# Kernel optimization log

Hardware: AMD Instinct MI355X
Metric: run time of the kernel (lower is better)

The kernel has to match this reference:

```python
import jax, jax.numpy as jnp
import numpy as np

B, C, T, F = 256, 1, 8192, 16


def _lrelu(h):
    return jnp.where(h > 0, h, 0.01 * h)


def _adain(h, style):
    # h: (B, T, 8), style: (B, 8, 2)
    scale = style[:, None, :, 0]          # (B, 1, 8)
    bias = style[:, None, :, 1]           # (B, 1, 8)
    mu = jnp.mean(h, axis=-1, keepdims=True)
    sigma = jnp.std(h, axis=-1, ddof=1, keepdims=True) + 1e-6  # torch.std is unbiased
    return scale * (h - mu) / sigma + bias


def setup_inputs() -> dict:
    key = jax.random.key(0)
    ks = jax.random.split(key, 20)
    g = lambda k, shp, s=0.2: (jax.random.normal(k, shp, dtype=jnp.float32) * s)
    inp = {
        "x": jax.random.normal(ks[0], (B, C, T), dtype=jnp.float32),
        "metadata": jax.random.normal(ks[1], (B, F), dtype=jnp.float32),
        # MetadataMLP: F->64->128->64 (total_channels*2 = 32*2)
        "mw1": g(ks[2], (F, 64)), "mb1": g(ks[3], (64,)),
        "mw2": g(ks[4], (64, 128)), "mb2": g(ks[5], (128,)),
        "mw3": g(ks[6], (128, 64)), "mb3": g(ks[7], (64,)),
        # main chain 1->8->8->8->8->1
        "w1": g(ks[8], (1, 8)), "b1": g(ks[9], (8,)),
        "w2": g(ks[10], (8, 8)), "b2": g(ks[11], (8,)),
        "w3": g(ks[12], (8, 8)), "b3": g(ks[13], (8,)),
        "w4": g(ks[14], (8, 8)), "b4": g(ks[15], (8,)),
        "w5": g(ks[16], (8, 1)), "b5": g(ks[17], (1,)),
    }
    return inp


def reference(x, metadata, mw1, mb1, mw2, mb2, mw3, mb3,
              w1, b1, w2, b2, w3, b3, w4, b4, w5, b5):
    # style MLP
    s = jax.nn.relu(metadata @ mw1 + mb1)
    s = jax.nn.relu(s @ mw2 + mb2)
    s = s @ mw3 + mb3                     # (B, 64)
    s1, s2, s3, s4 = jnp.split(s, 4, axis=1)  # each (B, 16)
    s1, s2, s3, s4 = (t.reshape(-1, 8, 2) for t in (s1, s2, s3, s4))

    h = jnp.transpose(x, (0, 2, 1))       # (B, T, 1)
    h = h @ w1 + b1                       # (B, T, 8)
    h = _lrelu(_adain(h, s1))
    h = h @ w2 + b2
    h = _lrelu(_adain(h, s2))
    h = h @ w3 + b3
    h = _lrelu(_adain(h, s3))
    h = h @ w4 + b4
    h = _lrelu(_adain(h, s4))
    h = h @ w5 + b5                       # (B, T, 1)
    out = _lrelu(h)
    return jnp.transpose(out, (0, 2, 1))  # (B, 1, T)
```

## Files before the change

kernel.cpp:

```cpp
#include <hip/hip_runtime.h>

#define BATCH   256
#define TLEN    8192
#define TPB     256
#define EPT     2
#define CHUNKS  (TLEN / (TPB * EPT))
#define PSTRIDE 320
#define SQRT7   2.6457513110645906f
#define C1      2.6457513110645906e-6f


__device__ __forceinline__ float rowmean8(const float* __restrict__ p) {
    return (((p[0] + p[1]) + (p[2] + p[3])) + ((p[4] + p[5]) + (p[6] + p[7]))) * 0.125f;
}

__device__ __forceinline__ float lrelu(float t) { return fmaxf(t, 0.01f * t); }

__global__ __launch_bounds__(128) void prep_kernel(
    const float* __restrict__ metadata,
    const float* __restrict__ mw1, const float* __restrict__ mb1,
    const float* __restrict__ mw2, const float* __restrict__ mb2,
    const float* __restrict__ mw3, const float* __restrict__ mb3,
    const float* __restrict__ w1, const float* __restrict__ b1,
    const float* __restrict__ w2, const float* __restrict__ b2,
    const float* __restrict__ w3, const float* __restrict__ b3,
    const float* __restrict__ w4, const float* __restrict__ b4,
    const float* __restrict__ w5, const float* __restrict__ b5,
    float* __restrict__ P)
{
    const int b   = blockIdx.x;
    const int tid = threadIdx.x;
    __shared__ float md[16];
    __shared__ float h1[64];
    __shared__ float h2[128];
    __shared__ float s[64];
    __shared__ float la[8], lc[8];

    if (tid < 16) md[tid] = metadata[b * 16 + tid];
    __syncthreads();

    if (tid < 64) {
        float a = mb1[tid];
        #pragma unroll
        for (int k = 0; k < 16; ++k) a = fmaf(md[k], mw1[k * 64 + tid], a);
        h1[tid] = fmaxf(a, 0.f);
    }
    __syncthreads();

    {
        float a = mb2[tid];
        #pragma unroll 16
        for (int k = 0; k < 64; ++k) a = fmaf(h1[k], mw2[k * 128 + tid], a);
        h2[tid] = fmaxf(a, 0.f);
    }
    __syncthreads();

    if (tid < 64) {
        float a = mb3[tid];
        #pragma unroll 16
        for (int k = 0; k < 128; ++k) a = fmaf(h2[k], mw3[k * 64 + tid], a);
        s[tid] = a;
    }
    if (tid >= 64 && tid < 72) {
        int j = tid - 64;
        la[j] = w1[j] - rowmean8(w1);
        lc[j] = b1[j] - rowmean8(b1);
    }
    __syncthreads();

    float* __restrict__ p = P + b * PSTRIDE;

    if (tid == 0) {
        float A = 0.f, B = 0.f, C = 0.f;
        #pragma unroll
        for (int j = 0; j < 8; ++j) {
            A = fmaf(la[j], la[j], A);
            B = fmaf(la[j], lc[j], B);
            C = fmaf(lc[j], lc[j], C);
        }
        p[24] = A; p[25] = 2.f * B; p[26] = C; p[27] = b5[0];
    }
    if (tid < 8) {
        const float sc1 = s[2 * tid] * SQRT7;
        p[tid]      = la[tid] * sc1;
        p[8 + tid]  = lc[tid] * sc1;
        p[16 + tid] = s[2 * tid + 1];
        p[32 + 64 + tid]  = b2[tid] - rowmean8(b2);
        p[32 + 72 + tid]  = s[16 + 2 * tid] * SQRT7;
        p[32 + 80 + tid]  = s[16 + 2 * tid + 1];
        p[120 + 64 + tid] = b3[tid] - rowmean8(b3);
        p[120 + 72 + tid] = s[32 + 2 * tid] * SQRT7;
        p[120 + 80 + tid] = s[32 + 2 * tid + 1];
        p[208 + 64 + tid] = b4[tid] - rowmean8(b4);
        p[208 + 72 + tid] = s[48 + 2 * tid] * SQRT7;
        p[208 + 80 + tid] = s[48 + 2 * tid + 1];
        p[296 + tid]      = w5[tid];
    }
    if (tid >= 64) {
        int i = tid - 64;
        p[32 + i]  = w2[i] - rowmean8(w2 + (i & 56));
        p[120 + i] = w3[i] - rowmean8(w3 + (i & 56));
        p[208 + i] = w4[i] - rowmean8(w4 + (i & 56));
    }
}

__global__ __launch_bounds__(TPB, 6) void adain_main_kernel(
    const float* __restrict__ x, const float* __restrict__ P, float* __restrict__ out)
{
    const int tid   = threadIdx.x;
    const int b     = blockIdx.x / CHUNKS;
    const int chunk = blockIdx.x % CHUNKS;

    const float* __restrict__ p = P + b * PSTRIDE;

    const float cA = p[24], cB2 = p[25], cC = p[26], lb5 = p[27];

    const int i2 = b * (TLEN / 2) + chunk * TPB + tid;
    const float2 v2 = ((const float2*)x)[i2];
    const float ve[2] = {v2.x, v2.y};
    float h[2][8];

    #pragma unroll
    for (int e = 0; e < 2; ++e) {
        const float var = fmaxf(fmaf(ve[e], fmaf(ve[e], cA, cB2), cC), 0.f);
        const float r   = __builtin_amdgcn_rcpf(__builtin_amdgcn_sqrtf(var) + C1);
        #pragma unroll
        for (int j = 0; j < 8; ++j) {
            const float d = fmaf(ve[e], p[j], p[8 + j]);
            h[e][j] = lrelu(fmaf(d, r, p[16 + j]));
        }
    }

    #pragma unroll
    for (int l = 0; l < 3; ++l) {
        const float* __restrict__ w = p + 32 + l * 88;

        float cbv[8], sbv[8];
        #pragma unroll
        for (int j = 0; j < 8; ++j) { cbv[j] = w[64 + j]; sbv[j] = w[80 + j]; }

        float g[2][8];
        #pragma unroll
        for (int e = 0; e < 2; ++e)
            #pragma unroll
            for (int j = 0; j < 8; ++j)
                g[e][j] = fmaf(h[e][0], w[j], cbv[j]);

        #pragma unroll
        for (int k = 1; k < 8; ++k)
            #pragma unroll
            for (int e = 0; e < 2; ++e)
                #pragma unroll
                for (int j = 0; j < 8; ++j)
                    g[e][j] = fmaf(h[e][k], w[k * 8 + j], g[e][j]);

        #pragma unroll
        for (int e = 0; e < 2; ++e) {
            float var = 0.f;
            #pragma unroll
            for (int j = 0; j < 8; ++j) var = fmaf(g[e][j], g[e][j], var);
            const float r = __builtin_amdgcn_rcpf(__builtin_amdgcn_sqrtf(var) + C1);
            #pragma unroll
            for (int j = 0; j < 8; ++j)
                h[e][j] = lrelu(fmaf(g[e][j] * r, w[72 + j], sbv[j]));
        }
    }

    float oe[2];
    #pragma unroll
    for (int e = 0; e < 2; ++e) {
        float a = lb5;
        #pragma unroll
        for (int k = 0; k < 8; ++k) a = fmaf(h[e][k], p[296 + k], a);
        oe[e] = lrelu(a);
    }
    ((float2*)out)[i2] = make_float2(oe[0], oe[1]);
}

extern "C" void kernel_launch(void* const* d_in, const int* in_sizes, int n_in,
                              void* d_out, int out_size, void* d_ws, size_t ws_size,
                              hipStream_t stream)
{
    const float* x        = (const float*)d_in[0];
    const float* metadata = (const float*)d_in[1];
    const float* mw1      = (const float*)d_in[2];
    const float* mb1      = (const float*)d_in[3];
    const float* mw2      = (const float*)d_in[4];
    const float* mb2      = (const float*)d_in[5];
    const float* mw3      = (const float*)d_in[6];
    const float* mb3      = (const float*)d_in[7];
    const float* w1       = (const float*)d_in[8];
    const float* b1       = (const float*)d_in[9];
    const float* w2       = (const float*)d_in[10];
    const float* b2       = (const float*)d_in[11];
    const float* w3       = (const float*)d_in[12];
    const float* b3       = (const float*)d_in[13];
    const float* w4       = (const float*)d_in[14];
    const float* b4       = (const float*)d_in[15];
    const float* w5       = (const float*)d_in[16];
    const float* b5       = (const float*)d_in[17];

    float* P = (float*)d_ws;

    prep_kernel<<<BATCH, 128, 0, stream>>>(
        metadata, mw1, mb1, mw2, mb2, mw3, mb3,
        w1, b1, w2, b2, w3, b3, w4, b4, w5, b5, P);
    adain_main_kernel<<<BATCH * CHUNKS, TPB, 0, stream>>>(x, P, (float*)d_out);
}
```

Baseline: 118.2 us.

## Stage per-batch params in LDS and process four elements per thread

Each thread now handles four timesteps loaded as a float4 instead of two. The per-batch parameter block is copied into shared memory once per block, and the weights are read as vectorized LDS loads. The layer loop is no longer unrolled and the occupancy hint drops from 6 to 4 blocks. The aim is fewer scalar/global parameter loads per element and wider memory transactions, at the cost of a block barrier, higher register pressure and fewer blocks in the grid.

```diff
diff --git a/kernel.cpp b/kernel.cpp
--- a/kernel.cpp
+++ b/kernel.cpp
@@ -3,7 +3,7 @@
 #define BATCH   256
 #define TLEN    8192
 #define TPB     256
-#define EPT     2
+#define EPT     4
 #define CHUNKS  (TLEN / (TPB * EPT))
 #define PSTRIDE 320
 #define SQRT7   2.6457513110645906f
@@ -104,24 +104,27 @@
     }
 }
 
-__global__ __launch_bounds__(TPB, 6) void adain_main_kernel(
+__global__ __launch_bounds__(TPB, 4) void adain_main_kernel(
     const float* __restrict__ x, const float* __restrict__ P, float* __restrict__ out)
 {
+    __shared__ float p[304];
+
     const int tid   = threadIdx.x;
     const int b     = blockIdx.x / CHUNKS;
     const int chunk = blockIdx.x % CHUNKS;
 
-    const float* __restrict__ p = P + b * PSTRIDE;
+    const int i4 = b * (TLEN / 4) + chunk * TPB + tid;
+    const float4 v = ((const float4*)x)[i4];
+
+    if (tid < 76) ((float4*)p)[tid] = ((const float4*)(P + b * PSTRIDE))[tid];
+    __syncthreads();
 
     const float cA = p[24], cB2 = p[25], cC = p[26], lb5 = p[27];
-
-    const int i2 = b * (TLEN / 2) + chunk * TPB + tid;
-    const float2 v2 = ((const float2*)x)[i2];
-    const float ve[2] = {v2.x, v2.y};
-    float h[2][8];
+    const float ve[4] = {v.x, v.y, v.z, v.w};
+    float h[4][8];
 
     #pragma unroll
-    for (int e = 0; e < 2; ++e) {
+    for (int e = 0; e < 4; ++e) {
         const float var = fmaxf(fmaf(ve[e], fmaf(ve[e], cA, cB2), cC), 0.f);
         const float r   = __builtin_amdgcn_rcpf(__builtin_amdgcn_sqrtf(var) + C1);
         #pragma unroll
@@ -131,50 +134,62 @@
         }
     }
 
-    #pragma unroll
+    #pragma unroll 1
     for (int l = 0; l < 3; ++l) {
         const float* __restrict__ w = p + 32 + l * 88;
 
-        float cbv[8], sbv[8];
-        #pragma unroll
-        for (int j = 0; j < 8; ++j) { cbv[j] = w[64 + j]; sbv[j] = w[80 + j]; }
-
-        float g[2][8];
-        #pragma unroll
-        for (int e = 0; e < 2; ++e)
-            #pragma unroll
-            for (int j = 0; j < 8; ++j)
-                g[e][j] = fmaf(h[e][0], w[j], cbv[j]);
-
-        #pragma unroll
-        for (int k = 1; k < 8; ++k)
-            #pragma unroll
-            for (int e = 0; e < 2; ++e)
-                #pragma unroll
-                for (int j = 0; j < 8; ++j)
-                    g[e][j] = fmaf(h[e][k], w[k * 8 + j], g[e][j]);
-
-        #pragma unroll
-        for (int e = 0; e < 2; ++e) {
+        float cb[8], sc[8], sb[8];
+        #pragma unroll
+        for (int j = 0; j < 8; ++j) { cb[j] = w[64 + j]; sc[j] = w[72 + j]; sb[j] = w[80 + j]; }
+
+        float g[4][8];
+        {
+            const float4 wa = *(const float4*)(w);
+            const float4 wb = *(const float4*)(w + 4);
+            #pragma unroll
+            for (int e = 0; e < 4; ++e) {
+                const float hk = h[e][0];
+                g[e][0] = fmaf(hk, wa.x, cb[0]); g[e][1] = fmaf(hk, wa.y, cb[1]);
+                g[e][2] = fmaf(hk, wa.z, cb[2]); g[e][3] = fmaf(hk, wa.w, cb[3]);
+                g[e][4] = fmaf(hk, wb.x, cb[4]); g[e][5] = fmaf(hk, wb.y, cb[5]);
+                g[e][6] = fmaf(hk, wb.z, cb[6]); g[e][7] = fmaf(hk, wb.w, cb[7]);
+            }
+        }
+        #pragma unroll
+        for (int k = 1; k < 8; ++k) {
+            const float4 wa = *(const float4*)(w + k * 8);
+            const float4 wb = *(const float4*)(w + k * 8 + 4);
+            #pragma unroll
+            for (int e = 0; e < 4; ++e) {
+                const float hk = h[e][k];
+                g[e][0] = fmaf(hk, wa.x, g[e][0]); g[e][1] = fmaf(hk, wa.y, g[e][1]);
+                g[e][2] = fmaf(hk, wa.z, g[e][2]); g[e][3] = fmaf(hk, wa.w, g[e][3]);
+                g[e][4] = fmaf(hk, wb.x, g[e][4]); g[e][5] = fmaf(hk, wb.y, g[e][5]);
+                g[e][6] = fmaf(hk, wb.z, g[e][6]); g[e][7] = fmaf(hk, wb.w, g[e][7]);
+            }
+        }
+
+        #pragma unroll
+        for (int e = 0; e < 4; ++e) {
             float var = 0.f;
             #pragma unroll
             for (int j = 0; j < 8; ++j) var = fmaf(g[e][j], g[e][j], var);
             const float r = __builtin_amdgcn_rcpf(__builtin_amdgcn_sqrtf(var) + C1);
             #pragma unroll
             for (int j = 0; j < 8; ++j)
-                h[e][j] = lrelu(fmaf(g[e][j] * r, w[72 + j], sbv[j]));
-        }
-    }
-
-    float oe[2];
+                h[e][j] = lrelu(fmaf(g[e][j] * r, sc[j], sb[j]));
+        }
+    }
+
+    float oe[4];
     #pragma unroll
-    for (int e = 0; e < 2; ++e) {
+    for (int e = 0; e < 4; ++e) {
         float a = lb5;
         #pragma unroll
         for (int k = 0; k < 8; ++k) a = fmaf(h[e][k], p[296 + k], a);
         oe[e] = lrelu(a);
     }
-    ((float2*)out)[i2] = make_float2(oe[0], oe[1]);
+    ((float4*)out)[i4] = make_float4(oe[0], oe[1], oe[2], oe[3]);
 }
 
 extern "C" void kernel_launch(void* const* d_in, const int* in_sizes, int n_in,
```

Result: faster. 114.9 us (-2.8%).
